# Kernel tuning notes

Measured on AMD Instinct MI355X. Metric: run time of the kernel, lower is better.

The kernel has to match this reference:

```python
import jax, jax.numpy as jnp
import numpy as np

B, S, D, H = 4, 2048, 1024, 16
HD = D // H  # head_dim = 64

def setup_inputs() -> dict:
    key = jax.random.key(0)
    ks = jax.random.split(key, 11)
    s = 1.0 / np.sqrt(D)
    return {
        "query": jax.random.normal(ks[0], (B, S, D), jnp.float32),
        "key": jax.random.normal(ks[1], (B, S, D), jnp.float32),
        "value": jax.random.normal(ks[2], (B, S, D), jnp.float32),
        "Wq": jax.random.normal(ks[3], (D, D), jnp.float32) * s,
        "bq": jnp.zeros((D,), jnp.float32),
        "Wk": jax.random.normal(ks[4], (D, D), jnp.float32) * s,
        "bk": jnp.zeros((D,), jnp.float32),
        "Wv": jax.random.normal(ks[5], (D, D), jnp.float32) * s,
        "bv": jnp.zeros((D,), jnp.float32),
        "Wo": jax.random.normal(ks[6], (D, D), jnp.float32) * s,
        "bo": jnp.zeros((D,), jnp.float32),
    }

def reference(query, key, value, Wq, bq, Wk, bk, Wv, bv, Wo, bo):
    b = query.shape[0]
    # linear projections, then split heads -> [b, H, S, HD]
    Q = (query @ Wq + bq).reshape(b, -1, H, HD).transpose(0, 2, 1, 3)
    K = (key @ Wk + bk).reshape(b, -1, H, HD).transpose(0, 2, 1, 3)
    V = (value @ Wv + bv).reshape(b, -1, H, HD).transpose(0, 2, 1, 3)
    energy = jnp.einsum('bhqd,bhkd->bhqk', Q, K) / np.sqrt(HD)  # [b,H,S,S]
    attn = jax.nn.softmax(energy, axis=-1)
    x = jnp.einsum('bhqk,bhkd->bhqd', attn, V)
    x = x.transpose(0, 2, 1, 3).reshape(b, -1, H * HD)
    return x @ Wo + bo
```

## Files before the change

kernel.cpp:

```cpp
#include <hip/hip_runtime.h>
#include <math.h>

constexpr int Bb = 4, Ss = 2048, Dd = 1024, Hh = 16, HDd = 64;

typedef __attribute__((ext_vector_type(8))) short short8;
typedef __attribute__((ext_vector_type(4))) float floatx4;
typedef __attribute__((ext_vector_type(16))) float floatx16;
typedef __attribute__((ext_vector_type(4))) unsigned int uint4v;

__device__ inline unsigned short bf16r(float f) {
    unsigned int u = __builtin_bit_cast(unsigned int, f);
    u += 0x7fffu + ((u >> 16) & 1u);
    return (unsigned short)(u >> 16);
}
__device__ inline unsigned int bf16pk2(float lo, float hi) {
    return (unsigned int)bf16r(lo) | ((unsigned int)bf16r(hi) << 16);
}
__device__ inline unsigned int cvtpk(float lo, float hi) {
    unsigned int r;
    asm("v_cvt_pk_bf16_f32 %0, %1, %2" : "=v"(r) : "v"(lo), "v"(hi));
    return r;
}
__device__ inline uint4v pk8(float4 x, float4 y) {
    uint4v r = {cvtpk(x.x, x.y), cvtpk(x.z, x.w), cvtpk(y.x, y.y), cvtpk(y.z, y.w)};
    return r;
}

__device__ inline void gld16(const void* g, void* l) {
    __builtin_amdgcn_global_load_lds((const __attribute__((address_space(1))) void*)g,
                                     (__attribute__((address_space(3))) void*)l, 16, 0, 0);
}

__device__ inline floatx4 mfma16(short8 a, short8 b, floatx4 c) {
    return __builtin_amdgcn_mfma_f32_16x16x32_bf16(a, b, c, 0, 0, 0);
}
__device__ inline floatx16 mfma32(short8 a, short8 b, floatx16 c) {
    return __builtin_amdgcn_mfma_f32_32x32x16_bf16(a, b, c, 0, 0, 0);
}

__global__ __launch_bounds__(256)
void conv_w_kernel(const float* __restrict__ Wq, const float* __restrict__ Wk,
                   const float* __restrict__ Wv, const float* __restrict__ Wo,
                   unsigned short* __restrict__ Wt)
{
    int z = blockIdx.z;
    const float* W = z == 0 ? Wq : z == 1 ? Wk : z == 2 ? Wv : Wo;
    float scale = z == 0 ? 0.125f : 1.0f;
    unsigned short* out = Wt + (size_t)z * 1024 * 1024;

    int r0 = blockIdx.x * 64;
    int c0 = blockIdx.y * 64;
    int t = threadIdx.x;
    int oc = (t & 3) * 16;
    int orow = c0 + (t >> 2);

    float v[16];
    #pragma unroll
    for (int j = 0; j < 16; ++j)
        v[j] = W[(size_t)(r0 + oc + j) * 1024 + orow] * scale;

    unsigned int pk[8];
    #pragma unroll
    for (int j = 0; j < 8; ++j) pk[j] = cvtpk(v[2 * j], v[2 * j + 1]);

    uint4v w0 = {pk[0], pk[1], pk[2], pk[3]};
    uint4v w1 = {pk[4], pk[5], pk[6], pk[7]};
    *(uint4v*)(out + (size_t)orow * 1024 + r0 + oc) = w0;
    *(uint4v*)(out + (size_t)orow * 1024 + r0 + oc + 8) = w1;
}

__global__ __launch_bounds__(256)
void conv_bias_kernel(const float* __restrict__ bq, float* __restrict__ bqs)
{
    int idx = blockIdx.x * 256 + threadIdx.x;
    if (idx < 1024) bqs[idx] = bq[idx] * 0.125f;
}

__global__ __launch_bounds__(256)
void qkv_gemm_kernel(const float* __restrict__ qin, const float* __restrict__ kin,
                     const float* __restrict__ vin,
                     const unsigned short* __restrict__ Wt,
                     const float* __restrict__ bqs, const float* __restrict__ bk,
                     const float* __restrict__ bv,
                     unsigned short* __restrict__ Qb, unsigned short* __restrict__ Kb,
                     unsigned short* __restrict__ Vb)
{
    int z = blockIdx.z;
    const float* A = z == 0 ? qin : z == 1 ? kin : vin;
    const unsigned short* W = Wt + (size_t)z * 1024 * 1024;
    const float* bias = z == 0 ? bqs : z == 1 ? bk : bv;
    unsigned short* O = z == 0 ? Qb : z == 1 ? Kb : Vb;

    __shared__ __align__(16) char qsm[36864];
    char* Asm0 = qsm;
    char* Bsm0 = qsm + 8192;
    char* Asm1 = qsm + 16384;
    char* Bsm1 = qsm + 24576;

    int tid = threadIdx.x, lane = tid & 63, w = tid >> 6;
    int wr = w >> 1, wc = w & 1;
    int fr = lane & 15, fg = lane >> 4;
    int m0 = blockIdx.x * 128, n0 = blockIdx.y * 128;

    const float* Arow = A + (size_t)(m0 + (tid >> 1)) * 1024 + (tid & 1) * 16;
    const int aWX = (tid & 4) << 2;
    const int aRdoB = (((wr * 64 + fr) * 32 + fg * 8) * 2) ^ ((fr & 2) << 3);
    const int bRdoB = ((wc * 64 + fr) * 32 + fg * 8) * 2;

    floatx4 acc[4][4] = {};

    {
        float4 a0 = *(const float4*)(Arow);
        float4 a1 = *(const float4*)(Arow + 4);
        float4 a2 = *(const float4*)(Arow + 8);
        float4 a3 = *(const float4*)(Arow + 12);
        char* pb = Asm0 + tid * 32;
        *(uint4v*)(pb + aWX) = pk8(a0, a1);
        *(uint4v*)(pb + (aWX ^ 16)) = pk8(a2, a3);
        #pragma unroll
        for (int it = 0; it < 2; ++it) {
            int cc = tid + it * 256;
            const unsigned short* gsrc = W + (size_t)(n0 + (cc >> 2)) * 1024 + (cc & 3) * 8;
            gld16(gsrc, Bsm0 + (size_t)(it * 256 + w * 64) * 16);
        }
    }
    __syncthreads();

    for (int kt = 0; kt < 32; ++kt) {
        char* Acur = (kt & 1) ? Asm1 : Asm0;
        char* Bcur = (kt & 1) ? Bsm1 : Bsm0;
        char* Anxt = (kt & 1) ? Asm0 : Asm1;
        char* Bnxt = (kt & 1) ? Bsm0 : Bsm1;

        float4 a0, a1, a2, a3;
        if (kt < 31) {
            const float* Ar = Arow + (kt + 1) * 32;
            a0 = *(const float4*)(Ar);
            a1 = *(const float4*)(Ar + 4);
            a2 = *(const float4*)(Ar + 8);
            a3 = *(const float4*)(Ar + 12);
            #pragma unroll
            for (int it = 0; it < 2; ++it) {
                int cc = tid + it * 256;
                const unsigned short* gsrc =
                    W + (size_t)(n0 + (cc >> 2)) * 1024 + (kt + 1) * 32 + (cc & 3) * 8;
                gld16(gsrc, Bnxt + (size_t)(it * 256 + w * 64) * 16);
            }
        }

        short8 af[4], bf[4];
        #pragma unroll
        for (int mi = 0; mi < 4; ++mi) af[mi] = *(const short8*)(Acur + aRdoB + mi * 1024);
        #pragma unroll
        for (int ni = 0; ni < 4; ++ni) bf[ni] = *(const short8*)(Bcur + bRdoB + ni * 1024);
        #pragma unroll
        for (int mi = 0; mi < 4; ++mi)
            #pragma unroll
            for (int ni = 0; ni < 4; ++ni)
                acc[mi][ni] = mfma16(af[mi], bf[ni], acc[mi][ni]);

        if (kt < 31) {
            char* pb = Anxt + tid * 32;
            *(uint4v*)(pb + aWX) = pk8(a0, a1);
            *(uint4v*)(pb + (aWX ^ 16)) = pk8(a2, a3);
        }
        __syncthreads();
    }

    float bvv[4];
    #pragma unroll
    for (int ni = 0; ni < 4; ++ni) bvv[ni] = bias[n0 + wc * 64 + ni * 16 + fr];

    if (z == 2) {
        unsigned short* T = (unsigned short*)(qsm) + (size_t)w * 4608;
        #pragma unroll
        for (int mi = 0; mi < 4; ++mi)
            #pragma unroll
            for (int ni = 0; ni < 4; ++ni) {
                int hdl = ni * 16 + fr;
                int sl  = mi * 16 + fg * 4;
                uint2 u2;
                u2.x = cvtpk(acc[mi][ni][0] + bvv[ni], acc[mi][ni][1] + bvv[ni]);
                u2.y = cvtpk(acc[mi][ni][2] + bvv[ni], acc[mi][ni][3] + bvv[ni]);
                *(uint2*)(T + hdl * 72 + sl) = u2;
            }
        int h  = (n0 + wc * 64) >> 6;
        int Ms = m0 + wr * 64;
        int b_ = Ms >> 11, sbase = Ms & 2047;
        unsigned short* Od = O + (((size_t)(b_ * 16 + h) * 64) << 11) + sbase;
        int rg = lane >> 3, sc = lane & 7;
        #pragma unroll
        for (int j = 0; j < 8; ++j) {
            int row = j * 8 + rg;
            uint4v t = *(const uint4v*)(T + row * 72 + sc * 8);
            *(uint4v*)(Od + ((size_t)row << 11) + sc * 8) = t;
        }
    } else {
        #pragma unroll
        for (int mi = 0; mi < 4; ++mi)
            #pragma unroll
            for (int ni = 0; ni < 4; ++ni) {
                int n = n0 + wc * 64 + ni * 16 + fr;
                int h = n >> 6, hd = n & 63;
                #pragma unroll
                for (int i = 0; i < 4; ++i) {
                    int m = m0 + wr * 64 + mi * 16 + fg * 4 + i;
                    int b_ = m >> 11, s = m & 2047;
                    float val = acc[mi][ni][i] + bvv[ni];
                    O[(((size_t)(b_ * 16 + h) * 2048 + s) << 6) + hd] = bf16r(val);
                }
            }
    }
}

__global__ __launch_bounds__(256)
void attn_kernel(const unsigned short* __restrict__ Qb, const unsigned short* __restrict__ Kb,
                 const unsigned short* __restrict__ Vtb, unsigned short* __restrict__ Xb)
{
    __shared__ __align__(16) char smem[33280];
    float* Ll = (float*)(smem + 32768);

    int tid = threadIdx.x, lane = tid & 63, w = tid >> 6;
    int c = lane & 31, hi = lane >> 5;
    int q0 = blockIdx.x * 128;
    size_t base = ((size_t)(blockIdx.z * 16 + blockIdx.y)) * 2048 * 64;
    const unsigned short* Qp = Qb + base + (size_t)(q0 + w * 32) * 64;
    const unsigned short* Kp = Kb + base;
    const unsigned short* Vp = Vtb + base;

    short8 qfr[4];
    #pragma unroll
    for (int ks = 0; ks < 4; ++ks)
        qfr[ks] = *(const short8*)(Qp + (size_t)c * 64 + ks * 16 + hi * 8);

    floatx16 acc_o[2] = {};
    float lsum = 0.f;

    int p0 = tid & 7;
    int r0 = tid >> 3;
    int r1 = r0 + 32;
    int g0 = p0 ^ (r0 & 7);

    auto STAGE = [&](int kt, char* Kd, char* Vd) {
        gld16(Kp + ((size_t)(kt * 64 + r0) << 6) + g0 * 8, Kd + (size_t)tid * 16);
        gld16(Kp + ((size_t)(kt * 64 + r1) << 6) + g0 * 8, Kd + (size_t)(tid + 256) * 16);
        gld16(Vp + ((size_t)r0 << 11) + kt * 64 + g0 * 8, Vd + (size_t)tid * 16);
        gld16(Vp + ((size_t)r1 << 11) + kt * 64 + g0 * 8, Vd + (size_t)(tid + 256) * 16);
    };

    STAGE(0, smem, smem + 8192);
    __syncthreads();

    for (int kt = 0; kt < 32; ++kt) {
        char* Kl = smem + (kt & 1) * 16384;
        char* Vl = Kl + 8192;
        if (kt + 1 < 32) {
            char* Kn = smem + ((kt + 1) & 1) * 16384;
            STAGE(kt + 1, Kn, Kn + 8192);
        }

        #pragma unroll
        for (int kvt = 0; kvt < 2; ++kvt) {
            floatx16 st = {};
            #pragma unroll
            for (int ks = 0; ks < 4; ++ks) {
                int row = kvt * 32 + c;
                short8 kf = *(const short8*)(Kl + row * 128 +
                                             ((ks * 32 + hi * 16) ^ ((row & 7) << 4)));
                st = mfma32(kf, qfr[ks], st);
            }

            float p[16];
            #pragma unroll
            for (int r = 0; r < 16; ++r) {
                p[r] = __expf(st[r] - 12.0f);
                lsum += p[r];
            }
            unsigned int j[8];
            #pragma unroll
            for (int t2 = 0; t2 < 8; ++t2)
                j[t2] = cvtpk(p[2 * t2], p[2 * t2 + 1]);
            unsigned int s0 = __shfl_xor(hi ? j[0] : j[2], 32, 64);
            unsigned int s1 = __shfl_xor(hi ? j[1] : j[3], 32, 64);
            unsigned int s2 = __shfl_xor(hi ? j[4] : j[6], 32, 64);
            unsigned int s3 = __shfl_xor(hi ? j[5] : j[7], 32, 64);
            uint4v pa0 = {hi ? s0 : j[0], hi ? s1 : j[1],
                          hi ? j[2] : s0, hi ? j[3] : s1};
            uint4v pa1 = {hi ? s2 : j[4], hi ? s3 : j[5],
                          hi ? j[6] : s2, hi ? j[7] : s3};
            short8 paA = __builtin_bit_cast(short8, pa0);
            short8 paB = __builtin_bit_cast(short8, pa1);

            #pragma unroll
            for (int kvs2 = 0; kvs2 < 2; ++kvs2) {
                int kstep = kvt * 2 + kvs2;
                short8 pa = kvs2 ? paB : paA;
                #pragma unroll
                for (int dvt = 0; dvt < 2; ++dvt) {
                    int dv = dvt * 32 + c;
                    short8 vf = *(const short8*)(Vl + dv * 128 +
                                                 ((kstep * 32 + hi * 16) ^ ((dv & 7) << 4)));
                    acc_o[dvt] = mfma32(pa, vf, acc_o[dvt]);
                }
            }
        }
        __syncthreads();
    }

    float ltot = lsum + __shfl_xor(lsum, 32, 64);
    if (hi == 0) Ll[w * 32 + c] = 1.0f / ltot;

    __syncthreads();
    unsigned short* Ot = (unsigned short*)smem;

    #pragma unroll
    for (int r = 0; r < 16; ++r) {
        int rowq = (r & 3) + 8 * (r >> 2) + 4 * hi;
        float inv = Ll[w * 32 + rowq];
        int ql = w * 32 + rowq;
        Ot[ql * 64 + c]      = bf16r(acc_o[0][r] * inv);
        Ot[ql * 64 + 32 + c] = bf16r(acc_o[1][r] * inv);
    }
    __syncthreads();

    {
        int row = tid >> 1, half = tid & 1;
        const unsigned short* src = Ot + row * 64 + half * 32;
        unsigned short* dst = Xb + ((size_t)blockIdx.z * 2048 + q0 + row) * 1024
                                 + blockIdx.y * 64 + half * 32;
        uint4v v0 = *(const uint4v*)(src);
        uint4v v1 = *(const uint4v*)(src + 8);
        uint4v v2 = *(const uint4v*)(src + 16);
        uint4v v3 = *(const uint4v*)(src + 24);
        *(uint4v*)(dst) = v0;
        *(uint4v*)(dst + 8) = v1;
        *(uint4v*)(dst + 16) = v2;
        *(uint4v*)(dst + 24) = v3;
    }
}

__global__ __launch_bounds__(256)
void out_gemm_kernel(const unsigned short* __restrict__ Xb,
                     const unsigned short* __restrict__ Wto,
                     const float* __restrict__ bo, float* __restrict__ out)
{
    __shared__ __align__(16) char osm[32768];
    unsigned short* Asm0 = (unsigned short*)(osm);
    unsigned short* Bsm0 = (unsigned short*)(osm + 8192);
    unsigned short* Asm1 = (unsigned short*)(osm + 16384);
    unsigned short* Bsm1 = (unsigned short*)(osm + 24576);

    int tid = threadIdx.x, lane = tid & 63, w = tid >> 6;
    int wr = w >> 1, wc = w & 1;
    int fr = lane & 15, fg = lane >> 4;
    int m0 = blockIdx.x * 128, n0 = blockIdx.y * 128;

    const int aRdo = (wr * 64 + fr) * 32 + fg * 8;
    const int bRdo = (wc * 64 + fr) * 32 + fg * 8;

    floatx4 acc[4][4] = {};

    auto STAGE = [&](int k0, unsigned short* Ad, unsigned short* Bd) {
        #pragma unroll
        for (int it = 0; it < 2; ++it) {
            int cA = tid + it * 256;
            const unsigned short* ga = Xb + (size_t)(m0 + (cA >> 2)) * 1024 + k0 + (cA & 3) * 8;
            gld16(ga, (char*)Ad + (size_t)(it * 256 + w * 64) * 16);
            const unsigned short* gb = Wto + (size_t)(n0 + (cA >> 2)) * 1024 + k0 + (cA & 3) * 8;
            gld16(gb, (char*)Bd + (size_t)(it * 256 + w * 64) * 16);
        }
    };

    STAGE(0, Asm0, Bsm0);
    __syncthreads();

    for (int kt = 0; kt < 32; ++kt) {
        unsigned short* Acur = (kt & 1) ? Asm1 : Asm0;
        unsigned short* Bcur = (kt & 1) ? Bsm1 : Bsm0;
        if (kt < 31)
            STAGE((kt + 1) * 32, (kt & 1) ? Asm0 : Asm1, (kt & 1) ? Bsm0 : Bsm1);

        short8 af[4], bf[4];
        #pragma unroll
        for (int mi = 0; mi < 4; ++mi) af[mi] = *(const short8*)(Acur + aRdo + mi * 16 * 32);
        #pragma unroll
        for (int ni = 0; ni < 4; ++ni) bf[ni] = *(const short8*)(Bcur + bRdo + ni * 16 * 32);
        #pragma unroll
        for (int mi = 0; mi < 4; ++mi)
            #pragma unroll
            for (int ni = 0; ni < 4; ++ni)
                acc[mi][ni] = mfma16(af[mi], bf[ni], acc[mi][ni]);
        __syncthreads();
    }

    float bvv[4];
    #pragma unroll
    for (int ni = 0; ni < 4; ++ni) bvv[ni] = bo[n0 + wc * 64 + ni * 16 + fr];

    #pragma unroll
    for (int mi = 0; mi < 4; ++mi)
        #pragma unroll
        for (int ni = 0; ni < 4; ++ni) {
            int n = n0 + wc * 64 + ni * 16 + fr;
            #pragma unroll
            for (int i = 0; i < 4; ++i) {
                int m = m0 + wr * 64 + mi * 16 + fg * 4 + i;
                out[(size_t)m * 1024 + n] = acc[mi][ni][i] + bvv[ni];
            }
        }
}

extern "C" void kernel_launch(void* const* d_in, const int* in_sizes, int n_in,
                              void* d_out, int out_size, void* d_ws, size_t ws_size,
                              hipStream_t stream)
{
    const float* qin = (const float*)d_in[0];
    const float* kin = (const float*)d_in[1];
    const float* vin = (const float*)d_in[2];
    const float* Wq  = (const float*)d_in[3];
    const float* bq  = (const float*)d_in[4];
    const float* Wk  = (const float*)d_in[5];
    const float* bk  = (const float*)d_in[6];
    const float* Wv  = (const float*)d_in[7];
    const float* bv  = (const float*)d_in[8];
    const float* Wo  = (const float*)d_in[9];
    const float* bo  = (const float*)d_in[10];
    float* out = (float*)d_out;

    char* ws = (char*)d_ws;
    unsigned short* Wt  = (unsigned short*)(ws);
    float*          bqs = (float*)(ws + 8388608);
    unsigned short* Qb  = (unsigned short*)(ws + 8392704);
    unsigned short* Kb  = (unsigned short*)(ws + 8392704 + 16777216);
    unsigned short* Vb  = (unsigned short*)(ws + 8392704 + 2 * 16777216);
    unsigned short* Xb  = (unsigned short*)(ws + 8392704 + 3 * 16777216);

    conv_w_kernel<<<dim3(16, 16, 4), 256, 0, stream>>>(Wq, Wk, Wv, Wo, Wt);
    conv_bias_kernel<<<dim3(4), 256, 0, stream>>>(bq, bqs);
    qkv_gemm_kernel<<<dim3(64, 8, 3), 256, 0, stream>>>(qin, kin, vin, Wt, bqs, bk, bv,
                                                        Qb, Kb, Vb);
    attn_kernel<<<dim3(16, 16, 4), 256, 0, stream>>>(Qb, Kb, Vb, Xb);
    out_gemm_kernel<<<dim3(64, 8), 256, 0, stream>>>(Xb, Wt + (size_t)3 * 1024 * 1024, bo, out);
}
```

Baseline: 236.1 us.

## Deepen QKV GEMM pipeline with triple-buffered weight tiles and partial waitcnt

Restructures the QKV projection main loop into a manually unrolled two-stage software pipeline. Weight tiles are triple-buffered in LDS via global_load_lds, and activation prefetches alternate between two register sets. Full __syncthreads is replaced by s_waitcnt vmcnt(6) plus s_barrier, so the loads for the next tile stay in flight while the current tile computes, hiding more global-load latency. It also shrinks the attention kernel's shared array and moves its row-sum scratch to offset 16384, which only works if the attention kernel uses no more than 16 KB for its other data.

After: 235.4 us. Within noise of the previous version (-0.3%).

```diff
diff --git a/kernel.cpp b/kernel.cpp
--- a/kernel.cpp
+++ b/kernel.cpp
@@ -12,9 +12,6 @@
     unsigned int u = __builtin_bit_cast(unsigned int, f);
     u += 0x7fffu + ((u >> 16) & 1u);
     return (unsigned short)(u >> 16);
-}
-__device__ inline unsigned int bf16pk2(float lo, float hi) {
-    return (unsigned int)bf16r(lo) | ((unsigned int)bf16r(hi) << 16);
 }
 __device__ inline unsigned int cvtpk(float lo, float hi) {
     unsigned int r;
@@ -91,11 +88,12 @@
     const float* bias = z == 0 ? bqs : z == 1 ? bk : bv;
     unsigned short* O = z == 0 ? Qb : z == 1 ? Kb : Vb;
 
-    __shared__ __align__(16) char qsm[36864];
-    char* Asm0 = qsm;
-    char* Bsm0 = qsm + 8192;
-    char* Asm1 = qsm + 16384;
-    char* Bsm1 = qsm + 24576;
+    __shared__ __align__(16) char qsm[40960];
+    char* Ab0 = qsm;
+    char* Ab1 = qsm + 8192;
+    char* pB0 = qsm + 16384;
+    char* pB1 = qsm + 24576;
+    char* pB2 = qsm + 32768;
 
     int tid = threadIdx.x, lane = tid & 63, w = tid >> 6;
     int wr = w >> 1, wc = w & 1;
@@ -108,64 +106,64 @@
     const int bRdoB = ((wc * 64 + fr) * 32 + fg * 8) * 2;
 
     floatx4 acc[4][4] = {};
-
-    {
-        float4 a0 = *(const float4*)(Arow);
-        float4 a1 = *(const float4*)(Arow + 4);
-        float4 a2 = *(const float4*)(Arow + 8);
-        float4 a3 = *(const float4*)(Arow + 12);
-        char* pb = Asm0 + tid * 32;
-        *(uint4v*)(pb + aWX) = pk8(a0, a1);
-        *(uint4v*)(pb + (aWX ^ 16)) = pk8(a2, a3);
-        #pragma unroll
-        for (int it = 0; it < 2; ++it) {
-            int cc = tid + it * 256;
-            const unsigned short* gsrc = W + (size_t)(n0 + (cc >> 2)) * 1024 + (cc & 3) * 8;
-            gld16(gsrc, Bsm0 + (size_t)(it * 256 + w * 64) * 16);
-        }
-    }
+    float4 arE0, arE1, arE2, arE3, arO0, arO1, arO2, arO3;
+
+#define LOADA(s, kt) { const float* Ar_ = Arow + (kt) * 32;                     \
+        s##0 = *(const float4*)(Ar_);      s##1 = *(const float4*)(Ar_ + 4);    \
+        s##2 = *(const float4*)(Ar_ + 8);  s##3 = *(const float4*)(Ar_ + 12); }
+#define GLB(kt, dst) {                                                          \
+        const unsigned short* g0_ = W + (size_t)(n0 + (tid >> 2)) * 1024 + (kt) * 32 + (tid & 3) * 8;          \
+        gld16(g0_, (dst) + (size_t)(w * 64) * 16);                              \
+        const unsigned short* g1_ = W + (size_t)(n0 + ((tid + 256) >> 2)) * 1024 + (kt) * 32 + (tid & 3) * 8;  \
+        gld16(g1_, (dst) + (size_t)(256 + w * 64) * 16); }
+#define WRITEA(s, dst) { char* pb_ = (dst) + tid * 32;                          \
+        *(uint4v*)(pb_ + aWX) = pk8(s##0, s##1);                                \
+        *(uint4v*)(pb_ + (aWX ^ 16)) = pk8(s##2, s##3); }
+#define COMP(Acur, Bcur) { short8 af_[4], bf_[4];                               \
+        _Pragma("unroll")                                                       \
+        for (int mi = 0; mi < 4; ++mi) af_[mi] = *(const short8*)((Acur) + aRdoB + mi * 1024); \
+        _Pragma("unroll")                                                       \
+        for (int ni = 0; ni < 4; ++ni) bf_[ni] = *(const short8*)((Bcur) + bRdoB + ni * 1024); \
+        _Pragma("unroll")                                                       \
+        for (int mi = 0; mi < 4; ++mi)                                          \
+            _Pragma("unroll")                                                   \
+            for (int ni = 0; ni < 4; ++ni)                                      \
+                acc[mi][ni] = mfma16(af_[mi], bf_[ni], acc[mi][ni]); }
+#define FENCE6 { asm volatile("s_waitcnt vmcnt(6) lgkmcnt(0)" ::: "memory");    \
+        __builtin_amdgcn_s_barrier(); __builtin_amdgcn_sched_barrier(0); }
+#define FENCE0 { asm volatile("s_waitcnt vmcnt(0) lgkmcnt(0)" ::: "memory");    \
+        __builtin_amdgcn_s_barrier(); __builtin_amdgcn_sched_barrier(0); }
+
+    LOADA(arE, 0); GLB(0, pB0);
+    LOADA(arO, 1); GLB(1, pB1);
+    WRITEA(arE, Ab0);
+    FENCE6;
+
+    for (int p = 0; p < 15; ++p) {
+        int kt = 2 * p;
+        LOADA(arE, kt + 2); GLB(kt + 2, pB2);
+        COMP(Ab0, pB0);
+        WRITEA(arO, Ab1);
+        FENCE6;
+        LOADA(arO, kt + 3); GLB(kt + 3, pB0);
+        COMP(Ab1, pB1);
+        WRITEA(arE, Ab0);
+        FENCE6;
+        char* t_ = pB0; pB0 = pB2; pB2 = pB1; pB1 = t_;
+    }
+
+    COMP(Ab0, pB0);
+    WRITEA(arO, Ab1);
+    FENCE0;
+    COMP(Ab1, pB1);
     __syncthreads();
 
-    for (int kt = 0; kt < 32; ++kt) {
-        char* Acur = (kt & 1) ? Asm1 : Asm0;
-        char* Bcur = (kt & 1) ? Bsm1 : Bsm0;
-        char* Anxt = (kt & 1) ? Asm0 : Asm1;
-        char* Bnxt = (kt & 1) ? Bsm0 : Bsm1;
-
-        float4 a0, a1, a2, a3;
-        if (kt < 31) {
-            const float* Ar = Arow + (kt + 1) * 32;
-            a0 = *(const float4*)(Ar);
-            a1 = *(const float4*)(Ar + 4);
-            a2 = *(const float4*)(Ar + 8);
-            a3 = *(const float4*)(Ar + 12);
-            #pragma unroll
-            for (int it = 0; it < 2; ++it) {
-                int cc = tid + it * 256;
-                const unsigned short* gsrc =
-                    W + (size_t)(n0 + (cc >> 2)) * 1024 + (kt + 1) * 32 + (cc & 3) * 8;
-                gld16(gsrc, Bnxt + (size_t)(it * 256 + w * 64) * 16);
-            }
-        }
-
-        short8 af[4], bf[4];
-        #pragma unroll
-        for (int mi = 0; mi < 4; ++mi) af[mi] = *(const short8*)(Acur + aRdoB + mi * 1024);
-        #pragma unroll
-        for (int ni = 0; ni < 4; ++ni) bf[ni] = *(const short8*)(Bcur + bRdoB + ni * 1024);
-        #pragma unroll
-        for (int mi = 0; mi < 4; ++mi)
-            #pragma unroll
-            for (int ni = 0; ni < 4; ++ni)
-                acc[mi][ni] = mfma16(af[mi], bf[ni], acc[mi][ni]);
-
-        if (kt < 31) {
-            char* pb = Anxt + tid * 32;
-            *(uint4v*)(pb + aWX) = pk8(a0, a1);
-            *(uint4v*)(pb + (aWX ^ 16)) = pk8(a2, a3);
-        }
-        __syncthreads();
-    }
+#undef LOADA
+#undef GLB
+#undef WRITEA
+#undef COMP
+#undef FENCE6
+#undef FENCE0
 
     float bvv[4];
     #pragma unroll
@@ -217,8 +215,8 @@
 void attn_kernel(const unsigned short* __restrict__ Qb, const unsigned short* __restrict__ Kb,
                  const unsigned short* __restrict__ Vtb, unsigned short* __restrict__ Xb)
 {
-    __shared__ __align__(16) char smem[33280];
-    float* Ll = (float*)(smem + 32768);
+    __shared__ __align__(16) char smem[32768];
+    float* Ll = (float*)(smem + 16384);
 
     int tid = threadIdx.x, lane = tid & 63, w = tid >> 6;
     int c = lane & 31, hi = lane >> 5;
```
